# Kernel optimization log

Hardware: AMD Instinct MI355X
Metric: run time of the kernel (lower is better)

The kernel has to match this reference:

```python
import jax, jax.numpy as jnp
import numpy as np

N_RUNS = 10  # neighborhoods_per_batch


def setup_inputs() -> dict:
    key = jax.random.key(0)
    k1, k2, k3 = jax.random.split(key, 3)
    B, U, NN, K = 128, 100000, 100, 500
    features = jax.random.normal(k1, (B, U), dtype=jnp.float32)
    positions = jax.random.uniform(k2, (U, 2), dtype=jnp.float32) * 10.0
    neighborhoods = jax.random.randint(k3, (NN, K), 0, U)
    return {"features": features, "positions": positions, "neighborhoods": neighborhoods}


def reference(features, positions, neighborhoods):
    # choose one random neighborhood per run (torch.randint equivalent, fixed key)
    choice = jax.random.randint(jax.random.key(42), (N_RUNS,), 0, neighborhoods.shape[0])
    idx = neighborhoods[choice]  # [n_runs, K]
    K = idx.shape[1]
    ii, jj = np.tril_indices(K, k=-1)  # strictly lower triangle pairs (i > j)

    def one_run(ind):
        nf = features[:, ind]        # [B, K] gathered neighborhood features
        npos = positions[ind]        # [K, 2]
        # pdist -> distance similarity 1/(d+1) over K*(K-1)/2 pairs
        d = jnp.linalg.norm(npos[ii] - npos[jj], axis=-1)
        dist_sim = 1.0 / (d + 1.0)
        # corrcoef of nf.T: rows are the K units (variables), B observations
        x = nf.T                     # [K, B]
        xc = x - x.mean(axis=1, keepdims=True)
        cov = xc @ xc.T              # [K, K]
        s = jnp.sqrt(jnp.diag(cov))
        corr = cov / (s[:, None] * s[None, :])
        resp_sim = corr[ii, jj]
        # pearson correlation between response and distance similarity vectors
        a = resp_sim - resp_sim.mean()
        b = dist_sim - dist_sim.mean()
        r = (a @ b) / (jnp.linalg.norm(a) * jnp.linalg.norm(b))
        return (1.0 - r) / 2.0

    losses = jax.vmap(one_run)(idx)  # vectorized over n_runs (no Python loop)
    return jnp.mean(losses)
```

## Files before the change

### kernel.cpp

```cpp
#include <hip/hip_runtime.h>
#include <hip/hip_bf16.h>
#include <stdint.h>

#define U_DIM 100000
#define B_DIM 128
#define K_DIM 500
#define NRUNS 10
#define KPAD  512
#define TILE  32
#define NTILES 16
#define NTILEPAIRS (NTILES * (NTILES + 1) / 2)
#define NPAIRWAVES (NTILEPAIRS * NRUNS)

typedef __attribute__((ext_vector_type(8))) short short8;
typedef __attribute__((ext_vector_type(4))) float f32x4;

struct ChoiceArgs { int c[NRUNS]; };

__global__ __launch_bounds__(256) void prep_kernel(
    const float* __restrict__ feat, const float* __restrict__ pos,
    const int* __restrict__ neigh, __hip_bfloat16* __restrict__ xnb,
    float2* __restrict__ npos, ChoiceArgs ch)
{
  int gw   = (blockIdx.x * 256 + threadIdx.x) >> 6;
  int lane = threadIdx.x & 63;
  if (gw >= NRUNS * K_DIM) return;
  int r = gw / K_DIM;
  int k = gw - r * K_DIM;

  int ind = neigh[ch.c[r] * K_DIM + k];
  float f0 = feat[(size_t)lane        * U_DIM + ind];
  float f1 = feat[(size_t)(lane + 64) * U_DIM + ind];

  float s  = f0 + f1;
  float ss = f0 * f0 + f1 * f1;
  #pragma unroll
  for (int off = 32; off; off >>= 1) {
    s  += __shfl_xor(s,  off);
    ss += __shfl_xor(ss, off);
  }
  float mean = s * (1.0f / 128.0f);
  float q    = ss - s * mean;
  float inv  = rsqrtf(q);

  size_t base = ((size_t)r * KPAD + k) * B_DIM;
  xnb[base + lane]      = __float2bfloat16((f0 - mean) * inv);
  xnb[base + lane + 64] = __float2bfloat16((f1 - mean) * inv);
  if (lane == 0) npos[r * KPAD + k] = make_float2(pos[2 * ind], pos[2 * ind + 1]);
}

__global__ __launch_bounds__(256) void pair_kernel(
    const __hip_bfloat16* __restrict__ xnb, const float2* __restrict__ npos,
    float* __restrict__ part)
{
  int gw   = (blockIdx.x * 256 + threadIdx.x) >> 6;
  int lane = threadIdx.x & 63;
  if (gw >= NPAIRWAVES) return;

  int r = gw / NTILEPAIRS;
  int p = gw - r * NTILEPAIRS;
  int ti = 0;
  while ((ti + 1) * (ti + 2) / 2 <= p) ti++;
  int tj = p - ti * (ti + 1) / 2;
  int i0 = ti * TILE, j0 = tj * TILE;

  const __hip_bfloat16* xr = xnb + (size_t)r * KPAD * B_DIM;
  int quad = lane >> 4, l16 = lane & 15;

  f32x4 acc00 = {}, acc01 = {}, acc10 = {}, acc11 = {};

  #pragma unroll
  for (int kk = 0; kk < 4; kk++) {
    int kb = kk * 32 + quad * 8;
    short8 a0 = *(const short8*)(xr + (size_t)(i0 + l16)      * B_DIM + kb);
    short8 a1 = *(const short8*)(xr + (size_t)(i0 + 16 + l16) * B_DIM + kb);
    short8 b0 = *(const short8*)(xr + (size_t)(j0 + l16)      * B_DIM + kb);
    short8 b1 = *(const short8*)(xr + (size_t)(j0 + 16 + l16) * B_DIM + kb);
    acc00 = __builtin_amdgcn_mfma_f32_16x16x32_bf16(a0, b0, acc00, 0, 0, 0);
    acc01 = __builtin_amdgcn_mfma_f32_16x16x32_bf16(a0, b1, acc01, 0, 0, 0);
    acc10 = __builtin_amdgcn_mfma_f32_16x16x32_bf16(a1, b0, acc10, 0, 0, 0);
    acc11 = __builtin_amdgcn_mfma_f32_16x16x32_bf16(a1, b1, acc11, 0, 0, 0);
  }

  const float2* pr = npos + r * KPAD;
  float sa = 0.f, sb = 0.f, saa = 0.f, sbb = 0.f, sab = 0.f;

  int gj0v = j0 + l16, gj1v = j0 + 16 + l16;
  float2 pj0 = pr[(gj0v < K_DIM) ? gj0v : 0];
  float2 pj1 = pr[(gj1v < K_DIM) ? gj1v : 0];

  #pragma unroll
  for (int tis = 0; tis < 2; tis++) {
    #pragma unroll
    for (int reg = 0; reg < 4; reg++) {
      int gi = i0 + tis * 16 + quad * 4 + reg;
      if (gi >= K_DIM) continue;
      float2 pi = pr[gi];
      if (gj0v < K_DIM && gi > gj0v) {
        float resp = tis ? acc10[reg] : acc00[reg];
        float dx = pi.x - pj0.x, dy = pi.y - pj0.y;
        float ds = 1.0f / (sqrtf(dx * dx + dy * dy) + 1.0f);
        sa += resp; sb += ds; saa += resp * resp; sbb += ds * ds; sab += resp * ds;
      }
      if (gj1v < K_DIM && gi > gj1v) {
        float resp = tis ? acc11[reg] : acc01[reg];
        float dx = pi.x - pj1.x, dy = pi.y - pj1.y;
        float ds = 1.0f / (sqrtf(dx * dx + dy * dy) + 1.0f);
        sa += resp; sb += ds; saa += resp * resp; sbb += ds * ds; sab += resp * ds;
      }
    }
  }

  #pragma unroll
  for (int off = 32; off; off >>= 1) {
    sa  += __shfl_xor(sa,  off);
    sb  += __shfl_xor(sb,  off);
    saa += __shfl_xor(saa, off);
    sbb += __shfl_xor(sbb, off);
    sab += __shfl_xor(sab, off);
  }

  if (lane == 0) {
    float* slot = part + (size_t)gw * 5;
    slot[0] = sa; slot[1] = sb; slot[2] = saa; slot[3] = sbb; slot[4] = sab;
  }
}

__global__ __launch_bounds__(640) void finalize_kernel(
    const float* __restrict__ part, float* __restrict__ out)
{
  __shared__ double contrib[NRUNS];
  int wave = threadIdx.x >> 6;
  int lane = threadIdx.x & 63;

  double v[5] = {0, 0, 0, 0, 0};
  for (int p = lane; p < NTILEPAIRS; p += 64) {
    const float* slot = part + ((size_t)wave * NTILEPAIRS + p) * 5;
    #pragma unroll
    for (int i = 0; i < 5; i++) v[i] += (double)slot[i];
  }
  #pragma unroll
  for (int off = 32; off; off >>= 1) {
    #pragma unroll
    for (int i = 0; i < 5; i++) v[i] += __shfl_xor(v[i], off);
  }
  if (lane == 0) {
    const double n = (double)(K_DIM * (K_DIM - 1) / 2);
    double cov = v[4] - v[0] * v[1] / n;
    double va  = v[2] - v[0] * v[0] / n;
    double vb  = v[3] - v[1] * v[1] / n;
    contrib[wave] = (1.0 - cov / sqrt(va * vb)) * 0.5;
  }
  __syncthreads();
  if (threadIdx.x == 0) {
    double total = 0.0;
    #pragma unroll
    for (int r = 0; r < NRUNS; r++) total += contrib[r];
    out[0] = (float)(total / NRUNS);
  }
}

static inline uint32_t rotl32_host(uint32_t x, int r) { return (x << r) | (x >> (32 - r)); }

static void tf2x32(uint32_t k0, uint32_t k1, uint32_t c0, uint32_t c1,
                   uint32_t& o0, uint32_t& o1)
{
  const uint32_t rots[2][4] = {{13, 15, 26, 6}, {17, 29, 16, 24}};
  uint32_t ks[3] = {k0, k1, k0 ^ k1 ^ 0x1BD11BDAu};
  uint32_t x0 = c0 + ks[0], x1 = c1 + ks[1];
  for (int i = 0; i < 5; i++) {
    const uint32_t* rr = rots[i & 1];
    for (int j = 0; j < 4; j++) {
      x0 += x1;
      x1 = rotl32_host(x1, (int)rr[j]);
      x1 ^= x0;
    }
    x0 += ks[(i + 1) % 3];
    x1 += ks[(i + 2) % 3] + (uint32_t)(i + 1);
  }
  o0 = x0; o1 = x1;
}

extern "C" void kernel_launch(void* const* d_in, const int* in_sizes, int n_in,
                              void* d_out, int out_size, void* d_ws, size_t ws_size,
                              hipStream_t stream)
{
  const float* feat  = (const float*)d_in[0];
  const float* pos   = (const float*)d_in[1];
  const int*   neigh = (const int*)d_in[2];
  float* out = (float*)d_out;

  ChoiceArgs ch;
  uint32_t A0, B0, A1, B1;
  tf2x32(0u, 42u, 0u, 2u, A0, B0);
  tf2x32(0u, 42u, 1u, 3u, A1, B1);
  uint32_t hi[NRUNS], lo[NRUNS];
  for (int e = 0; e < 5; e++) {
    uint32_t h0, h1, l0, l1;
    tf2x32(A0, A1, (uint32_t)e, (uint32_t)(e + 5), h0, h1);
    hi[e] = h0; hi[e + 5] = h1;
    tf2x32(B0, B1, (uint32_t)e, (uint32_t)(e + 5), l0, l1);
    lo[e] = l0; lo[e + 5] = l1;
  }
  for (int e = 0; e < NRUNS; e++)
    ch.c[e] = (int)(((hi[e] % 100u) * 96u + (lo[e] % 100u)) % 100u);

  char* ws = (char*)d_ws;
  __hip_bfloat16* xnb = (__hip_bfloat16*)ws;
  size_t off0 = (size_t)NRUNS * KPAD * B_DIM * sizeof(__hip_bfloat16);
  float2* npos = (float2*)(ws + off0);
  float*  part = (float*)(ws + off0 + (size_t)NRUNS * KPAD * sizeof(float2));

  prep_kernel<<<dim3((NRUNS * K_DIM) / 4), 256, 0, stream>>>(feat, pos, neigh, xnb, npos, ch);
  pair_kernel<<<dim3(NPAIRWAVES / 4), 256, 0, stream>>>(xnb, npos, part);
  finalize_kernel<<<dim3(1), 640, 0, stream>>>(part, out);
}
```

Measured before the change: 102.4 us.

## Fuse prep, pair and finalize into one cooperative kernel and dedupe runs

Merges the three kernels into a single cooperative kernel separated by grid-wide syncs, with grid-stride loops over gather and tile-pair work. Duplicate neighborhood choices are merged on the host with weights so repeated runs are computed once. Pair tiles shrink from 32x32 to 16x16 to spread work over more waves. The grid syncs add cost, and the larger partial-sum buffer relies on the workspace being big enough.

```diff
diff --git a/kernel.cpp b/kernel.cpp
--- a/kernel.cpp
+++ b/kernel.cpp
@@ -1,162 +1,149 @@
 #include <hip/hip_runtime.h>
+#include <hip/hip_cooperative_groups.h>
 #include <hip/hip_bf16.h>
 #include <stdint.h>
+
+namespace cg = cooperative_groups;
 
 #define U_DIM 100000
 #define B_DIM 128
 #define K_DIM 500
 #define NRUNS 10
 #define KPAD  512
-#define TILE  32
-#define NTILES 16
-#define NTILEPAIRS (NTILES * (NTILES + 1) / 2)
-#define NPAIRWAVES (NTILEPAIRS * NRUNS)
+#define T16   16
+#define NT16  32
+#define NTP16 (NT16 * (NT16 + 1) / 2)
+
+#define GRID_BLOCKS   1024
+#define BLOCK_THREADS 256
+#define NWAVES (GRID_BLOCKS * BLOCK_THREADS / 64)
 
 typedef __attribute__((ext_vector_type(8))) short short8;
 typedef __attribute__((ext_vector_type(4))) float f32x4;
 
-struct ChoiceArgs { int c[NRUNS]; };
-
-__global__ __launch_bounds__(256) void prep_kernel(
+struct Args { int c[NRUNS]; float w[NRUNS]; int ru; };
+
+__global__ __launch_bounds__(BLOCK_THREADS) void fused_kernel(
     const float* __restrict__ feat, const float* __restrict__ pos,
-    const int* __restrict__ neigh, __hip_bfloat16* __restrict__ xnb,
-    float2* __restrict__ npos, ChoiceArgs ch)
+    const int* __restrict__ neigh, float* __restrict__ out,
+    __hip_bfloat16* __restrict__ xnb, float2* __restrict__ npos,
+    float* __restrict__ part, Args a)
 {
-  int gw   = (blockIdx.x * 256 + threadIdx.x) >> 6;
+  cg::grid_group grid = cg::this_grid();
+  int gw   = (blockIdx.x * BLOCK_THREADS + threadIdx.x) >> 6;
   int lane = threadIdx.x & 63;
-  if (gw >= NRUNS * K_DIM) return;
-  int r = gw / K_DIM;
-  int k = gw - r * K_DIM;
-
-  int ind = neigh[ch.c[r] * K_DIM + k];
-  float f0 = feat[(size_t)lane        * U_DIM + ind];
-  float f1 = feat[(size_t)(lane + 64) * U_DIM + ind];
-
-  float s  = f0 + f1;
-  float ss = f0 * f0 + f1 * f1;
-  #pragma unroll
-  for (int off = 32; off; off >>= 1) {
-    s  += __shfl_xor(s,  off);
-    ss += __shfl_xor(ss, off);
-  }
-  float mean = s * (1.0f / 128.0f);
-  float q    = ss - s * mean;
-  float inv  = rsqrtf(q);
-
-  size_t base = ((size_t)r * KPAD + k) * B_DIM;
-  xnb[base + lane]      = __float2bfloat16((f0 - mean) * inv);
-  xnb[base + lane + 64] = __float2bfloat16((f1 - mean) * inv);
-  if (lane == 0) npos[r * KPAD + k] = make_float2(pos[2 * ind], pos[2 * ind + 1]);
-}
-
-__global__ __launch_bounds__(256) void pair_kernel(
-    const __hip_bfloat16* __restrict__ xnb, const float2* __restrict__ npos,
-    float* __restrict__ part)
-{
-  int gw   = (blockIdx.x * 256 + threadIdx.x) >> 6;
-  int lane = threadIdx.x & 63;
-  if (gw >= NPAIRWAVES) return;
-
-  int r = gw / NTILEPAIRS;
-  int p = gw - r * NTILEPAIRS;
-  int ti = 0;
-  while ((ti + 1) * (ti + 2) / 2 <= p) ti++;
-  int tj = p - ti * (ti + 1) / 2;
-  int i0 = ti * TILE, j0 = tj * TILE;
-
-  const __hip_bfloat16* xr = xnb + (size_t)r * KPAD * B_DIM;
+
+  int totC = a.ru * KPAD;
+  for (int c = gw; c < totC; c += NWAVES) {
+    int r = c >> 9;
+    int k = c & (KPAD - 1);
+    size_t base = ((size_t)r * KPAD + k) * B_DIM;
+    if (k < K_DIM) {
+      int ind = neigh[a.c[r] * K_DIM + k];
+      float f0 = feat[(size_t)lane        * U_DIM + ind];
+      float f1 = feat[(size_t)(lane + 64) * U_DIM + ind];
+      float s  = f0 + f1;
+      float ss = f0 * f0 + f1 * f1;
+      #pragma unroll
+      for (int off = 32; off; off >>= 1) {
+        s  += __shfl_xor(s,  off);
+        ss += __shfl_xor(ss, off);
+      }
+      float mean = s * (1.0f / 128.0f);
+      float q    = ss - s * mean;
+      float inv  = rsqrtf(q);
+      xnb[base + lane]      = __float2bfloat16((f0 - mean) * inv);
+      xnb[base + lane + 64] = __float2bfloat16((f1 - mean) * inv);
+      if (lane == 0) npos[r * KPAD + k] = make_float2(pos[2 * ind], pos[2 * ind + 1]);
+    } else {
+      xnb[base + lane]      = __float2bfloat16(0.0f);
+      xnb[base + lane + 64] = __float2bfloat16(0.0f);
+    }
+  }
+
+  grid.sync();
+
+  int totP = a.ru * NTP16;
   int quad = lane >> 4, l16 = lane & 15;
-
-  f32x4 acc00 = {}, acc01 = {}, acc10 = {}, acc11 = {};
-
-  #pragma unroll
-  for (int kk = 0; kk < 4; kk++) {
-    int kb = kk * 32 + quad * 8;
-    short8 a0 = *(const short8*)(xr + (size_t)(i0 + l16)      * B_DIM + kb);
-    short8 a1 = *(const short8*)(xr + (size_t)(i0 + 16 + l16) * B_DIM + kb);
-    short8 b0 = *(const short8*)(xr + (size_t)(j0 + l16)      * B_DIM + kb);
-    short8 b1 = *(const short8*)(xr + (size_t)(j0 + 16 + l16) * B_DIM + kb);
-    acc00 = __builtin_amdgcn_mfma_f32_16x16x32_bf16(a0, b0, acc00, 0, 0, 0);
-    acc01 = __builtin_amdgcn_mfma_f32_16x16x32_bf16(a0, b1, acc01, 0, 0, 0);
-    acc10 = __builtin_amdgcn_mfma_f32_16x16x32_bf16(a1, b0, acc10, 0, 0, 0);
-    acc11 = __builtin_amdgcn_mfma_f32_16x16x32_bf16(a1, b1, acc11, 0, 0, 0);
-  }
-
-  const float2* pr = npos + r * KPAD;
-  float sa = 0.f, sb = 0.f, saa = 0.f, sbb = 0.f, sab = 0.f;
-
-  int gj0v = j0 + l16, gj1v = j0 + 16 + l16;
-  float2 pj0 = pr[(gj0v < K_DIM) ? gj0v : 0];
-  float2 pj1 = pr[(gj1v < K_DIM) ? gj1v : 0];
-
-  #pragma unroll
-  for (int tis = 0; tis < 2; tis++) {
+  for (int item = gw; item < totP; item += NWAVES) {
+    int r = item / NTP16;
+    int p = item - r * NTP16;
+    int ti = 0;
+    while ((ti + 1) * (ti + 2) / 2 <= p) ti++;
+    int tj = p - ti * (ti + 1) / 2;
+    int i0 = ti * T16, j0 = tj * T16;
+
+    const __hip_bfloat16* xr = xnb + (size_t)r * KPAD * B_DIM;
+    f32x4 acc = {};
+    #pragma unroll
+    for (int kk = 0; kk < 4; kk++) {
+      int kb = kk * 32 + quad * 8;
+      short8 av = *(const short8*)(xr + (size_t)(i0 + l16) * B_DIM + kb);
+      short8 bv = *(const short8*)(xr + (size_t)(j0 + l16) * B_DIM + kb);
+      acc = __builtin_amdgcn_mfma_f32_16x16x32_bf16(av, bv, acc, 0, 0, 0);
+    }
+
+    const float2* pr = npos + r * KPAD;
+    int gj = j0 + l16;
+    float2 pj = pr[(gj < K_DIM) ? gj : 0];
+    float sa = 0.f, sb = 0.f, saa = 0.f, sbb = 0.f, sab = 0.f;
     #pragma unroll
     for (int reg = 0; reg < 4; reg++) {
-      int gi = i0 + tis * 16 + quad * 4 + reg;
-      if (gi >= K_DIM) continue;
-      float2 pi = pr[gi];
-      if (gj0v < K_DIM && gi > gj0v) {
-        float resp = tis ? acc10[reg] : acc00[reg];
-        float dx = pi.x - pj0.x, dy = pi.y - pj0.y;
+      int gi = i0 + quad * 4 + reg;
+      if (gi < K_DIM && gj < K_DIM && gi > gj) {
+        float resp = acc[reg];
+        float2 pi = pr[gi];
+        float dx = pi.x - pj.x, dy = pi.y - pj.y;
         float ds = 1.0f / (sqrtf(dx * dx + dy * dy) + 1.0f);
         sa += resp; sb += ds; saa += resp * resp; sbb += ds * ds; sab += resp * ds;
       }
-      if (gj1v < K_DIM && gi > gj1v) {
-        float resp = tis ? acc11[reg] : acc01[reg];
-        float dx = pi.x - pj1.x, dy = pi.y - pj1.y;
-        float ds = 1.0f / (sqrtf(dx * dx + dy * dy) + 1.0f);
-        sa += resp; sb += ds; saa += resp * resp; sbb += ds * ds; sab += resp * ds;
-      }
-    }
-  }
-
-  #pragma unroll
-  for (int off = 32; off; off >>= 1) {
-    sa  += __shfl_xor(sa,  off);
-    sb  += __shfl_xor(sb,  off);
-    saa += __shfl_xor(saa, off);
-    sbb += __shfl_xor(sbb, off);
-    sab += __shfl_xor(sab, off);
-  }
-
-  if (lane == 0) {
-    float* slot = part + (size_t)gw * 5;
-    slot[0] = sa; slot[1] = sb; slot[2] = saa; slot[3] = sbb; slot[4] = sab;
-  }
-}
-
-__global__ __launch_bounds__(640) void finalize_kernel(
-    const float* __restrict__ part, float* __restrict__ out)
-{
-  __shared__ double contrib[NRUNS];
-  int wave = threadIdx.x >> 6;
-  int lane = threadIdx.x & 63;
-
-  double v[5] = {0, 0, 0, 0, 0};
-  for (int p = lane; p < NTILEPAIRS; p += 64) {
-    const float* slot = part + ((size_t)wave * NTILEPAIRS + p) * 5;
+    }
+
     #pragma unroll
-    for (int i = 0; i < 5; i++) v[i] += (double)slot[i];
-  }
-  #pragma unroll
-  for (int off = 32; off; off >>= 1) {
-    #pragma unroll
-    for (int i = 0; i < 5; i++) v[i] += __shfl_xor(v[i], off);
-  }
-  if (lane == 0) {
-    const double n = (double)(K_DIM * (K_DIM - 1) / 2);
-    double cov = v[4] - v[0] * v[1] / n;
-    double va  = v[2] - v[0] * v[0] / n;
-    double vb  = v[3] - v[1] * v[1] / n;
-    contrib[wave] = (1.0 - cov / sqrt(va * vb)) * 0.5;
-  }
-  __syncthreads();
-  if (threadIdx.x == 0) {
-    double total = 0.0;
-    #pragma unroll
-    for (int r = 0; r < NRUNS; r++) total += contrib[r];
-    out[0] = (float)(total / NRUNS);
+    for (int off = 32; off; off >>= 1) {
+      sa  += __shfl_xor(sa,  off);
+      sb  += __shfl_xor(sb,  off);
+      saa += __shfl_xor(saa, off);
+      sbb += __shfl_xor(sbb, off);
+      sab += __shfl_xor(sab, off);
+    }
+    if (lane == 0) {
+      float* slot = part + (size_t)item * 5;
+      slot[0] = sa; slot[1] = sb; slot[2] = saa; slot[3] = sbb; slot[4] = sab;
+    }
+  }
+
+  grid.sync();
+
+  if (blockIdx.x == 0) {
+    __shared__ double contrib[NRUNS];
+    int wv = threadIdx.x >> 6;
+    for (int r = wv; r < a.ru; r += BLOCK_THREADS / 64) {
+      double v[5] = {0, 0, 0, 0, 0};
+      for (int p = lane; p < NTP16; p += 64) {
+        const float* slot = part + ((size_t)r * NTP16 + p) * 5;
+        #pragma unroll
+        for (int i = 0; i < 5; i++) v[i] += (double)slot[i];
+      }
+      #pragma unroll
+      for (int off = 32; off; off >>= 1) {
+        #pragma unroll
+        for (int i = 0; i < 5; i++) v[i] += __shfl_xor(v[i], off);
+      }
+      if (lane == 0) {
+        const double n = (double)(K_DIM * (K_DIM - 1) / 2);
+        double cov = v[4] - v[0] * v[1] / n;
+        double va  = v[2] - v[0] * v[0] / n;
+        double vb  = v[3] - v[1] * v[1] / n;
+        contrib[r] = (double)a.w[r] * (1.0 - cov / sqrt(va * vb)) * 0.5;
+      }
+    }
+    __syncthreads();
+    if (threadIdx.x == 0) {
+      double total = 0.0;
+      for (int r = 0; r < a.ru; r++) total += contrib[r];
+      out[0] = (float)(total / NRUNS);
+    }
   }
 }
 
@@ -190,7 +177,6 @@
   const int*   neigh = (const int*)d_in[2];
   float* out = (float*)d_out;
 
-  ChoiceArgs ch;
   uint32_t A0, B0, A1, B1;
   tf2x32(0u, 42u, 0u, 2u, A0, B0);
   tf2x32(0u, 42u, 1u, 3u, A1, B1);
@@ -202,8 +188,18 @@
     tf2x32(B0, B1, (uint32_t)e, (uint32_t)(e + 5), l0, l1);
     lo[e] = l0; lo[e + 5] = l1;
   }
-  for (int e = 0; e < NRUNS; e++)
-    ch.c[e] = (int)(((hi[e] % 100u) * 96u + (lo[e] % 100u)) % 100u);
+
+  Args ar;
+  for (int e = 0; e < NRUNS; e++) { ar.c[e] = 0; ar.w[e] = 0.0f; }
+  int ru = 0;
+  for (int e = 0; e < NRUNS; e++) {
+    int cv = (int)(((hi[e] % 100u) * 96u + (lo[e] % 100u)) % 100u);
+    int f = -1;
+    for (int u = 0; u < ru; u++) if (ar.c[u] == cv) { f = u; break; }
+    if (f >= 0) ar.w[f] += 1.0f;
+    else { ar.c[ru] = cv; ar.w[ru] = 1.0f; ru++; }
+  }
+  ar.ru = ru;
 
   char* ws = (char*)d_ws;
   __hip_bfloat16* xnb = (__hip_bfloat16*)ws;
@@ -211,7 +207,8 @@
   float2* npos = (float2*)(ws + off0);
   float*  part = (float*)(ws + off0 + (size_t)NRUNS * KPAD * sizeof(float2));
 
-  prep_kernel<<<dim3((NRUNS * K_DIM) / 4), 256, 0, stream>>>(feat, pos, neigh, xnb, npos, ch);
-  pair_kernel<<<dim3(NPAIRWAVES / 4), 256, 0, stream>>>(xnb, npos, part);
-  finalize_kernel<<<dim3(1), 640, 0, stream>>>(part, out);
+  void* params[] = { (void*)&feat, (void*)&pos, (void*)&neigh, (void*)&out,
+                     (void*)&xnb, (void*)&npos, (void*)&part, (void*)&ar };
+  hipLaunchCooperativeKernel((void*)fused_kernel, dim3(GRID_BLOCKS),
+                             dim3(BLOCK_THREADS), params, 0, stream);
 }
```

Result: slower. 321.2 us (+213.8%).

## Deduplicate repeated neighborhood choices and fuse finalize into pair kernel

Applied to the files above, without the earlier changes.

The host now deduplicates the chosen neighborhood indices and computes each unique run once, weighting its loss by its multiplicity. The finalize kernel is removed; the last pair wave, detected with a global atomic counter, reduces all partials and writes the output. It also zero-pads the unused KPAD rows and starts the tile-pair index from a sqrt-based estimate. The intent is to skip redundant work and save one kernel launch, at the cost of a serial single-wave final reduction and an atomic/fence handshake.

```diff
diff --git a/kernel.cpp b/kernel.cpp
--- a/kernel.cpp
+++ b/kernel.cpp
@@ -10,25 +10,32 @@
 #define TILE  32
 #define NTILES 16
 #define NTILEPAIRS (NTILES * (NTILES + 1) / 2)
-#define NPAIRWAVES (NTILEPAIRS * NRUNS)
 
 typedef __attribute__((ext_vector_type(8))) short short8;
 typedef __attribute__((ext_vector_type(4))) float f32x4;
 
-struct ChoiceArgs { int c[NRUNS]; };
+struct Args { int c[NRUNS]; float w[NRUNS]; int ru; };
 
 __global__ __launch_bounds__(256) void prep_kernel(
     const float* __restrict__ feat, const float* __restrict__ pos,
     const int* __restrict__ neigh, __hip_bfloat16* __restrict__ xnb,
-    float2* __restrict__ npos, ChoiceArgs ch)
+    float2* __restrict__ npos, unsigned* __restrict__ done_ctr, Args a)
 {
   int gw   = (blockIdx.x * 256 + threadIdx.x) >> 6;
   int lane = threadIdx.x & 63;
-  if (gw >= NRUNS * K_DIM) return;
-  int r = gw / K_DIM;
-  int k = gw - r * K_DIM;
-
-  int ind = neigh[ch.c[r] * K_DIM + k];
+  if (blockIdx.x == 0 && threadIdx.x == 0) *done_ctr = 0u;
+  if (gw >= a.ru * KPAD) return;
+  int r = gw >> 9;
+  int k = gw & (KPAD - 1);
+
+  size_t base = ((size_t)r * KPAD + k) * B_DIM;
+  if (k >= K_DIM) {
+    xnb[base + lane]      = __float2bfloat16(0.0f);
+    xnb[base + lane + 64] = __float2bfloat16(0.0f);
+    return;
+  }
+
+  int ind = neigh[a.c[r] * K_DIM + k];
   float f0 = feat[(size_t)lane        * U_DIM + ind];
   float f1 = feat[(size_t)(lane + 64) * U_DIM + ind];
 
@@ -43,7 +50,6 @@
   float q    = ss - s * mean;
   float inv  = rsqrtf(q);
 
-  size_t base = ((size_t)r * KPAD + k) * B_DIM;
   xnb[base + lane]      = __float2bfloat16((f0 - mean) * inv);
   xnb[base + lane + 64] = __float2bfloat16((f1 - mean) * inv);
   if (lane == 0) npos[r * KPAD + k] = make_float2(pos[2 * ind], pos[2 * ind + 1]);
@@ -51,16 +57,19 @@
 
 __global__ __launch_bounds__(256) void pair_kernel(
     const __hip_bfloat16* __restrict__ xnb, const float2* __restrict__ npos,
-    float* __restrict__ part)
+    float* __restrict__ part, float* __restrict__ out,
+    unsigned* __restrict__ done_ctr, Args a)
 {
   int gw   = (blockIdx.x * 256 + threadIdx.x) >> 6;
   int lane = threadIdx.x & 63;
-  if (gw >= NPAIRWAVES) return;
+  int total = a.ru * NTILEPAIRS;
+  if (gw >= total) return;
 
   int r = gw / NTILEPAIRS;
   int p = gw - r * NTILEPAIRS;
-  int ti = 0;
+  int ti = (int)((sqrtf(8.0f * (float)p + 1.0f) - 1.0f) * 0.5f);
   while ((ti + 1) * (ti + 2) / 2 <= p) ti++;
+  while (ti * (ti + 1) / 2 > p) ti--;
   int tj = p - ti * (ti + 1) / 2;
   int i0 = ti * TILE, j0 = tj * TILE;
 
@@ -68,7 +77,6 @@
   int quad = lane >> 4, l16 = lane & 15;
 
   f32x4 acc00 = {}, acc01 = {}, acc10 = {}, acc11 = {};
-
   #pragma unroll
   for (int kk = 0; kk < 4; kk++) {
     int kb = kk * 32 + quad * 8;
@@ -84,7 +92,6 @@
 
   const float2* pr = npos + r * KPAD;
   float sa = 0.f, sb = 0.f, saa = 0.f, sbb = 0.f, sab = 0.f;
-
   int gj0v = j0 + l16, gj1v = j0 + 16 + l16;
   float2 pj0 = pr[(gj0v < K_DIM) ? gj0v : 0];
   float2 pj1 = pr[(gj1v < K_DIM) ? gj1v : 0];
@@ -119,45 +126,40 @@
     sbb += __shfl_xor(sbb, off);
     sab += __shfl_xor(sab, off);
   }
-
   if (lane == 0) {
     float* slot = part + (size_t)gw * 5;
     slot[0] = sa; slot[1] = sb; slot[2] = saa; slot[3] = sbb; slot[4] = sab;
   }
-}
-
-__global__ __launch_bounds__(640) void finalize_kernel(
-    const float* __restrict__ part, float* __restrict__ out)
-{
-  __shared__ double contrib[NRUNS];
-  int wave = threadIdx.x >> 6;
-  int lane = threadIdx.x & 63;
-
-  double v[5] = {0, 0, 0, 0, 0};
-  for (int p = lane; p < NTILEPAIRS; p += 64) {
-    const float* slot = part + ((size_t)wave * NTILEPAIRS + p) * 5;
+
+  __threadfence();
+  unsigned old = 0;
+  if (lane == 0) old = atomicAdd(done_ctr, 1u);
+  old = __shfl(old, 0);
+  if (old != (unsigned)(total - 1)) return;
+
+  __threadfence();
+  double tloss = 0.0;
+  for (int rr = 0; rr < a.ru; rr++) {
+    double v[5] = {0, 0, 0, 0, 0};
+    for (int pp = lane; pp < NTILEPAIRS; pp += 64) {
+      const float* slot = part + ((size_t)rr * NTILEPAIRS + pp) * 5;
+      #pragma unroll
+      for (int i = 0; i < 5; i++) v[i] += (double)slot[i];
+    }
     #pragma unroll
-    for (int i = 0; i < 5; i++) v[i] += (double)slot[i];
-  }
-  #pragma unroll
-  for (int off = 32; off; off >>= 1) {
-    #pragma unroll
-    for (int i = 0; i < 5; i++) v[i] += __shfl_xor(v[i], off);
-  }
-  if (lane == 0) {
-    const double n = (double)(K_DIM * (K_DIM - 1) / 2);
-    double cov = v[4] - v[0] * v[1] / n;
-    double va  = v[2] - v[0] * v[0] / n;
-    double vb  = v[3] - v[1] * v[1] / n;
-    contrib[wave] = (1.0 - cov / sqrt(va * vb)) * 0.5;
-  }
-  __syncthreads();
-  if (threadIdx.x == 0) {
-    double total = 0.0;
-    #pragma unroll
-    for (int r = 0; r < NRUNS; r++) total += contrib[r];
-    out[0] = (float)(total / NRUNS);
-  }
+    for (int off = 32; off; off >>= 1) {
+      #pragma unroll
+      for (int i = 0; i < 5; i++) v[i] += __shfl_xor(v[i], off);
+    }
+    if (lane == 0) {
+      const double n = (double)(K_DIM * (K_DIM - 1) / 2);
+      double cov = v[4] - v[0] * v[1] / n;
+      double va  = v[2] - v[0] * v[0] / n;
+      double vb  = v[3] - v[1] * v[1] / n;
+      tloss += (double)a.w[rr] * (1.0 - cov / sqrt(va * vb)) * 0.5;
+    }
+  }
+  if (lane == 0) out[0] = (float)(tloss / NRUNS);
 }
 
 static inline uint32_t rotl32_host(uint32_t x, int r) { return (x << r) | (x >> (32 - r)); }
@@ -190,7 +192,6 @@
   const int*   neigh = (const int*)d_in[2];
   float* out = (float*)d_out;
 
-  ChoiceArgs ch;
   uint32_t A0, B0, A1, B1;
   tf2x32(0u, 42u, 0u, 2u, A0, B0);
   tf2x32(0u, 42u, 1u, 3u, A1, B1);
@@ -202,16 +203,29 @@
     tf2x32(B0, B1, (uint32_t)e, (uint32_t)(e + 5), l0, l1);
     lo[e] = l0; lo[e + 5] = l1;
   }
-  for (int e = 0; e < NRUNS; e++)
-    ch.c[e] = (int)(((hi[e] % 100u) * 96u + (lo[e] % 100u)) % 100u);
+
+  Args ar;
+  for (int e = 0; e < NRUNS; e++) { ar.c[e] = 0; ar.w[e] = 0.0f; }
+  int ru = 0;
+  for (int e = 0; e < NRUNS; e++) {
+    int cv = (int)(((hi[e] % 100u) * 96u + (lo[e] % 100u)) % 100u);
+    int f = -1;
+    for (int u = 0; u < ru; u++) if (ar.c[u] == cv) { f = u; break; }
+    if (f >= 0) ar.w[f] += 1.0f;
+    else { ar.c[ru] = cv; ar.w[ru] = 1.0f; ru++; }
+  }
+  ar.ru = ru;
 
   char* ws = (char*)d_ws;
   __hip_bfloat16* xnb = (__hip_bfloat16*)ws;
   size_t off0 = (size_t)NRUNS * KPAD * B_DIM * sizeof(__hip_bfloat16);
   float2* npos = (float2*)(ws + off0);
-  float*  part = (float*)(ws + off0 + (size_t)NRUNS * KPAD * sizeof(float2));
-
-  prep_kernel<<<dim3((NRUNS * K_DIM) / 4), 256, 0, stream>>>(feat, pos, neigh, xnb, npos, ch);
-  pair_kernel<<<dim3(NPAIRWAVES / 4), 256, 0, stream>>>(xnb, npos, part);
-  finalize_kernel<<<dim3(1), 640, 0, stream>>>(part, out);
-}
+  size_t off1 = off0 + (size_t)NRUNS * KPAD * sizeof(float2);
+  float*  part = (float*)(ws + off1);
+  unsigned* done_ctr = (unsigned*)(ws + off1 + (size_t)NRUNS * NTILEPAIRS * 5 * sizeof(float));
+
+  int prep_waves = ru * KPAD;
+  int pair_waves = ru * NTILEPAIRS;
+  prep_kernel<<<dim3((prep_waves + 3) / 4), 256, 0, stream>>>(feat, pos, neigh, xnb, npos, done_ctr, ar);
+  pair_kernel<<<dim3((pair_waves + 3) / 4), 256, 0, stream>>>(xnb, npos, part, out, done_ctr, ar);
+}
```

Result: slower. 147.0 us (+43.6%).
